# Optimization experiments

Hardware: AMD Instinct MI355X
Metric: run time of the kernel (lower is better)

The kernel has to match this reference:

```python
import jax, jax.numpy as jnp
import numpy as np

EMBED = 768
HEADS = 12


def setup_inputs() -> dict:
    key = jax.random.key(0)
    k1, k2, k3 = jax.random.split(key, 3)
    B, N, E = 2, 2048, EMBED
    x = jax.random.normal(k1, (B, N, E), dtype=jnp.float32)
    w_qkv = jax.random.normal(k2, (3 * E, E), dtype=jnp.float32) * (1.0 / np.sqrt(E))
    b_qkv = jnp.zeros((3 * E,), dtype=jnp.float32)
    w_o = jax.random.normal(k3, (E, E), dtype=jnp.float32) * (1.0 / np.sqrt(E))
    b_o = jnp.zeros((E,), dtype=jnp.float32)
    return {"x": x, "w_qkv": w_qkv, "b_qkv": b_qkv, "w_o": w_o, "b_o": b_o}


def reference(x, w_qkv, b_qkv, w_o, b_o):
    B, N, E = x.shape
    H = HEADS
    d = E // H
    # fused qkv projection (torch Linear: x @ W^T + b)
    qkv = x @ w_qkv.T + b_qkv                       # [B, N, 3E]
    # Rearrange 'b n (h qkv e) -> b qkv h n e'
    qkv = qkv.reshape(B, N, H, 3, d).transpose(0, 3, 2, 1, 4)  # [B, 3, H, N, d]
    q, k, v = qkv[:, 0], qkv[:, 1], qkv[:, 2]       # each [B, H, N, d]
    scores = jnp.einsum("bhqd,bhkd->bhqk", q, k)    # [B, H, N, N]
    attn = jax.nn.softmax(scores / jnp.sqrt(jnp.float32(E)), axis=-1)
    ctx = jnp.einsum("bhqk,bhkd->bhqd", attn, v)    # [B, H, N, d]
    ctx = ctx.transpose(0, 2, 1, 3).reshape(B, N, E)  # 'b h n d -> b n (h d)'
    out = ctx @ w_o.T + b_o
    return out
```

## Files before the change

### kernel.cpp

```cpp
#include <hip/hip_runtime.h>

#define BB 2
#define NN 2048
#define EE 768
#define HH 12
#define DD 64
#define MM (BB*NN)
#define E3 (3*EE)
#define QSCALE 0.05205877280961602f

typedef __bf16 bf16x8 __attribute__((ext_vector_type(8)));
typedef float  f32x4  __attribute__((ext_vector_type(4)));
typedef unsigned short u16x8 __attribute__((ext_vector_type(8)));

#define MFMA(a,b,c) __builtin_amdgcn_mfma_f32_16x16x32_bf16(a,b,c,0,0,0)

__device__ __forceinline__ unsigned short f2bf(float f) {
    unsigned int u = __float_as_uint(f);
    u += 0x7FFFu + ((u >> 16) & 1u);
    return (unsigned short)(u >> 16);
}

typedef __attribute__((address_space(3))) unsigned int as3u32;
typedef __attribute__((address_space(1))) unsigned int as1u32;
__device__ __forceinline__ void gll16(const void* g, void* l) {
    __builtin_amdgcn_global_load_lds((const as1u32*)(uintptr_t)g,
                                     (as3u32*)(unsigned int)(uintptr_t)l, 16, 0, 0);
}

#define XB4 786432
#define WQ4 442368
#define WO4 147456
__global__ __launch_bounds__(256)
void cast3(const float* __restrict__ x, const float* __restrict__ wq,
           const float* __restrict__ wo, unsigned short* __restrict__ dst) {
    int i = blockIdx.x * 256 + threadIdx.x;
    const float* src;
    int off;
    if (i < XB4)            { src = x;  off = i; }
    else if (i < XB4+WQ4)   { src = wq; off = i - XB4; }
    else                    { src = wo; off = i - XB4 - WQ4; }
    float4 v = ((const float4*)src)[off];
    ushort4 o;
    o.x = f2bf(v.x); o.y = f2bf(v.y); o.z = f2bf(v.z); o.w = f2bf(v.w);
    ((ushort4*)dst)[i] = o;
}

__global__ __launch_bounds__(256)
void gemm_qkv(const unsigned short* __restrict__ A, const unsigned short* __restrict__ W,
              const float* __restrict__ bias,
              unsigned short* __restrict__ o0, unsigned short* __restrict__ o1,
              unsigned short* __restrict__ o2)
{
    __shared__ unsigned short As[256 * 32];
    __shared__ unsigned short Bs[128 * 32];

    const int tid = threadIdx.x;
    const int l = tid & 63;
    const int w = tid >> 6;
    const int m0 = blockIdx.x * 256;
    const int c0 = blockIdx.y * 128;
    const int wm = (w >> 1) * 128;
    const int wn = (w & 1) * 64;

    const unsigned short* a_src[4];
    const unsigned short* b_src[2];
    unsigned short* a_dst[4];
    unsigned short* b_dst[2];
    #pragma unroll
    for (int s = 0; s < 4; ++s) {
        a_src[s] = A + (size_t)(m0 + w*64 + s*16 + (l>>2)) * EE + (l&3)*8;
        a_dst[s] = &As[(w*64 + s*16) * 32];
    }
    #pragma unroll
    for (int s = 0; s < 2; ++s) {
        b_src[s] = W + (size_t)(c0 + w*32 + s*16 + (l>>2)) * EE + (l&3)*8;
        b_dst[s] = &Bs[(w*32 + s*16) * 32];
    }

    const f32x4 zero4 = {0.f, 0.f, 0.f, 0.f};
    f32x4 acc[8][4];
    #pragma unroll
    for (int i = 0; i < 8; ++i)
        #pragma unroll
        for (int j = 0; j < 4; ++j) acc[i][j] = zero4;

    for (int k0 = 0; k0 < EE; k0 += 32) {
        __syncthreads();
        #pragma unroll
        for (int s = 0; s < 4; ++s) gll16(a_src[s] + k0, a_dst[s]);
        #pragma unroll
        for (int s = 0; s < 2; ++s) gll16(b_src[s] + k0, b_dst[s]);
        __syncthreads();

        bf16x8 af[8], bf[4];
        #pragma unroll
        for (int i = 0; i < 8; ++i)
            af[i] = *(const bf16x8*)&As[(wm + 16*i + (l&15))*32 + (l>>4)*8];
        #pragma unroll
        for (int j = 0; j < 4; ++j)
            bf[j] = *(const bf16x8*)&Bs[(wn + 16*j + (l&15))*32 + (l>>4)*8];
        #pragma unroll
        for (int i = 0; i < 8; ++i)
            #pragma unroll
            for (int j = 0; j < 4; ++j)
                acc[i][j] = MFMA(af[i], bf[j], acc[i][j]);
    }

    const int sec = (c0 + wn) >> 6;
    const int hh = sec / 3;
    const int tt = sec - hh*3;
    #pragma unroll
    for (int j = 0; j < 4; ++j) {
        const int col = c0 + wn + 16*j + (l&15);
        const int dcol = 16*j + (l&15);
        const float bj = bias[col];
        #pragma unroll
        for (int i = 0; i < 8; ++i) {
            const int row0 = m0 + wm + 16*i + (l>>4)*4;
            const int b = row0 >> 11;
            const int n = row0 & (NN - 1);
            if (tt == 2) {
                ushort4 pk;
                pk.x = f2bf(acc[i][j][0] + bj);
                pk.y = f2bf(acc[i][j][1] + bj);
                pk.z = f2bf(acc[i][j][2] + bj);
                pk.w = f2bf(acc[i][j][3] + bj);
                *(ushort4*)&o2[(((size_t)b*HH + hh)*DD + dcol)*NN + n] = pk;
            } else {
                unsigned short* dst = (tt == 0) ? o0 : o1;
                #pragma unroll
                for (int r = 0; r < 4; ++r) {
                    float val = acc[i][j][r] + bj;
                    if (tt == 0) val *= QSCALE;
                    dst[(((size_t)b*HH + hh)*NN + n + r)*DD + dcol] = f2bf(val);
                }
            }
        }
    }
}

__global__ __launch_bounds__(256)
void gemm_out(const unsigned short* __restrict__ A, const unsigned short* __restrict__ W,
              const float* __restrict__ bias, float* __restrict__ of)
{
    __shared__ unsigned short As[128 * 32];
    __shared__ unsigned short Bs[128 * 32];

    const int tid = threadIdx.x;
    const int l = tid & 63;
    const int w = tid >> 6;
    const int m0 = blockIdx.x * 128;
    const int c0 = blockIdx.y * 128;
    const int wm = (w >> 1) * 64;
    const int wn = (w & 1) * 64;

    const int s0 = w * 2;
    const unsigned short* a_src0 = A + (size_t)(m0 + s0*16      + (l>>2)) * EE + (l&3)*8;
    const unsigned short* a_src1 = A + (size_t)(m0 + (s0+1)*16  + (l>>2)) * EE + (l&3)*8;
    const unsigned short* b_src0 = W + (size_t)(c0 + s0*16      + (l>>2)) * EE + (l&3)*8;
    const unsigned short* b_src1 = W + (size_t)(c0 + (s0+1)*16  + (l>>2)) * EE + (l&3)*8;
    unsigned short* a_dst0 = &As[s0*512];
    unsigned short* a_dst1 = &As[(s0+1)*512];
    unsigned short* b_dst0 = &Bs[s0*512];
    unsigned short* b_dst1 = &Bs[(s0+1)*512];

    const f32x4 zero4 = {0.f, 0.f, 0.f, 0.f};
    f32x4 acc[4][4];
    #pragma unroll
    for (int i = 0; i < 4; ++i)
        #pragma unroll
        for (int j = 0; j < 4; ++j) acc[i][j] = zero4;

    for (int k0 = 0; k0 < EE; k0 += 32) {
        __syncthreads();
        gll16(a_src0 + k0, a_dst0);
        gll16(a_src1 + k0, a_dst1);
        gll16(b_src0 + k0, b_dst0);
        gll16(b_src1 + k0, b_dst1);
        __syncthreads();

        bf16x8 af[4], bf[4];
        #pragma unroll
        for (int i = 0; i < 4; ++i)
            af[i] = *(const bf16x8*)&As[(wm + 16*i + (l&15))*32 + (l>>4)*8];
        #pragma unroll
        for (int j = 0; j < 4; ++j)
            bf[j] = *(const bf16x8*)&Bs[(wn + 16*j + (l&15))*32 + (l>>4)*8];
        #pragma unroll
        for (int i = 0; i < 4; ++i)
            #pragma unroll
            for (int j = 0; j < 4; ++j)
                acc[i][j] = MFMA(af[i], bf[j], acc[i][j]);
    }

    #pragma unroll
    for (int j = 0; j < 4; ++j) {
        const int col = c0 + wn + 16*j + (l&15);
        const float bj = bias[col];
        #pragma unroll
        for (int i = 0; i < 4; ++i) {
            #pragma unroll
            for (int r = 0; r < 4; ++r) {
                const int row = m0 + wm + 16*i + (l>>4)*4 + r;
                of[(size_t)row * EE + col] = acc[i][j][r] + bj;
            }
        }
    }
}

__global__ __launch_bounds__(256)
void attn_mfma(const unsigned short* __restrict__ Q, const unsigned short* __restrict__ K,
               const unsigned short* __restrict__ Vt_g, unsigned short* __restrict__ ctx)
{
    __shared__ unsigned short Ks[64 * 72];
    __shared__ unsigned short Vt[64 * 72];
    __shared__ unsigned short Pq[4 * 16 * 72];

    const int tid = threadIdx.x;
    const int l = tid & 63;
    const int w = tid >> 6;
    const int quad = l >> 4;
    const int lc = l & 15;

    const int id = blockIdx.x;
    const int bh = id % 24;
    const int bq = id / 24;
    const int b  = bh / 12;
    const int h  = bh - b*12;
    const size_t hb = (size_t)bh * NN * DD;

    const f32x4 zero4 = {0.f, 0.f, 0.f, 0.f};

    const int qrow = bq*64 + w*16 + lc;
    const bf16x8 qf0 = *(const bf16x8*)(Q + hb + (size_t)qrow*DD +      quad*8);
    const bf16x8 qf1 = *(const bf16x8*)(Q + hb + (size_t)qrow*DD + 32 + quad*8);

    f32x4 o[4];
    #pragma unroll
    for (int dj = 0; dj < 4; ++dj) o[dj] = zero4;
    float lsum = 0.f;

    const int srow = tid >> 2;
    const int sc = tid & 3;
    const unsigned short* kbase = K + hb + (size_t)srow*DD + sc*16;
    const unsigned short* vbase = Vt_g + ((size_t)bh*DD + srow)*NN + sc*16;
    unsigned short* ksl = &Ks[srow*72 + sc*16];
    unsigned short* vsl = &Vt[srow*72 + sc*16];

    for (int kt = 0; kt < NN/64; ++kt) {
        const unsigned short* ksrc = kbase + (size_t)kt*64*DD;
        const unsigned short* vsrc = vbase + kt*64;
        u16x8 k0 = *(const u16x8*)ksrc;
        u16x8 k1 = *(const u16x8*)(ksrc + 8);
        u16x8 v0 = *(const u16x8*)vsrc;
        u16x8 v1 = *(const u16x8*)(vsrc + 8);
        __syncthreads();
        *(u16x8*)ksl = k0;
        *(u16x8*)(ksl + 8) = k1;
        *(u16x8*)vsl = v0;
        *(u16x8*)(vsl + 8) = v1;
        __syncthreads();

        f32x4 st[4];
        #pragma unroll
        for (int jf = 0; jf < 4; ++jf) {
            bf16x8 kf0 = *(const bf16x8*)&Ks[(16*jf + lc)*72 +      quad*8];
            bf16x8 kf1 = *(const bf16x8*)&Ks[(16*jf + lc)*72 + 32 + quad*8];
            f32x4 acc0 = MFMA(kf0, qf0, zero4);
            st[jf] = MFMA(kf1, qf1, acc0);
        }

        #pragma unroll
        for (int jf = 0; jf < 4; ++jf) {
            float e0 = __builtin_amdgcn_exp2f(st[jf][0]);
            float e1 = __builtin_amdgcn_exp2f(st[jf][1]);
            float e2 = __builtin_amdgcn_exp2f(st[jf][2]);
            float e3 = __builtin_amdgcn_exp2f(st[jf][3]);
            lsum += (e0 + e1) + (e2 + e3);
            ushort4 pk;
            pk.x = f2bf(e0); pk.y = f2bf(e1); pk.z = f2bf(e2); pk.w = f2bf(e3);
            *(ushort4*)&Pq[w*1152 + lc*72 + 16*jf + quad*4] = pk;
        }

        #pragma unroll
        for (int kb = 0; kb < 2; ++kb) {
            bf16x8 pf = *(const bf16x8*)&Pq[w*1152 + lc*72 + kb*32 + quad*8];
            #pragma unroll
            for (int dj = 0; dj < 4; ++dj) {
                bf16x8 vf = *(const bf16x8*)&Vt[(16*dj + lc)*72 + kb*32 + quad*8];
                o[dj] = MFMA(vf, pf, o[dj]);
            }
        }
    }

    lsum += __shfl_xor(lsum, 16);
    lsum += __shfl_xor(lsum, 32);
    const float inv = 1.f / lsum;

    const int n = bq*64 + w*16 + lc;
    #pragma unroll
    for (int dj = 0; dj < 4; ++dj) {
        ushort4 pk;
        pk.x = f2bf(o[dj][0] * inv);
        pk.y = f2bf(o[dj][1] * inv);
        pk.z = f2bf(o[dj][2] * inv);
        pk.w = f2bf(o[dj][3] * inv);
        *(ushort4*)&ctx[((size_t)(b*NN + n))*EE + h*DD + 16*dj + quad*4] = pk;
    }
}

extern "C" void kernel_launch(void* const* d_in, const int* in_sizes, int n_in,
                              void* d_out, int out_size, void* d_ws, size_t ws_size,
                              hipStream_t stream)
{
    const float* x     = (const float*)d_in[0];
    const float* w_qkv = (const float*)d_in[1];
    const float* b_qkv = (const float*)d_in[2];
    const float* w_o   = (const float*)d_in[3];
    const float* b_o   = (const float*)d_in[4];
    float* out = (float*)d_out;

    unsigned short* wsu = (unsigned short*)d_ws;
    const size_t XB = (size_t)MM * EE;
    const size_t WQ = (size_t)E3 * EE;
    const size_t WO = (size_t)EE * EE;
    const size_t HS = (size_t)BB * HH * NN * DD;
    unsigned short* xb   = wsu;
    unsigned short* wqb  = xb  + XB;
    unsigned short* wob  = wqb + WQ;
    unsigned short* qb   = wob + WO;
    unsigned short* kb   = qb  + HS;
    unsigned short* vtb  = kb  + HS;
    unsigned short* ctxb = vtb + HS;

    cast3<<<(XB4 + WQ4 + WO4)/256, 256, 0, stream>>>(x, w_qkv, w_o, xb);

    dim3 g1(MM/256, E3/128);
    gemm_qkv<<<g1, 256, 0, stream>>>(xb, wqb, b_qkv, qb, kb, vtb);

    attn_mfma<<<768, 256, 0, stream>>>(qb, kb, vtb, ctxb);

    dim3 g3(MM/128, EE/128);
    gemm_out<<<g3, 256, 0, stream>>>(ctxb, wob, b_o, out);
}
```

Baseline: 204.5 us.

## Shrink GEMM tiles for more blocks and XOR-swizzle attention LDS layout

The QKV GEMM tile drops from 256x128 to 128x128 and the output GEMM tile from 128x128 to 64x128, which doubles the grid sizes to fill more CUs. The attention kernel replaces padded (stride 72) shared-memory rows with unpadded 64-wide rows and XOR swizzles on K, Vt and P tiles to avoid bank conflicts while using less LDS. Smaller GEMM tiles give lower arithmetic reuse per block and more global traffic.

```diff
diff --git a/kernel.cpp b/kernel.cpp
--- a/kernel.cpp
+++ b/kernel.cpp
@@ -52,56 +52,51 @@
               unsigned short* __restrict__ o0, unsigned short* __restrict__ o1,
               unsigned short* __restrict__ o2)
 {
-    __shared__ unsigned short As[256 * 32];
+    __shared__ unsigned short As[128 * 32];
     __shared__ unsigned short Bs[128 * 32];
 
     const int tid = threadIdx.x;
     const int l = tid & 63;
     const int w = tid >> 6;
-    const int m0 = blockIdx.x * 256;
+    const int m0 = blockIdx.x * 128;
     const int c0 = blockIdx.y * 128;
-    const int wm = (w >> 1) * 128;
+    const int wm = (w >> 1) * 64;
     const int wn = (w & 1) * 64;
 
-    const unsigned short* a_src[4];
-    const unsigned short* b_src[2];
-    unsigned short* a_dst[4];
-    unsigned short* b_dst[2];
-    #pragma unroll
-    for (int s = 0; s < 4; ++s) {
-        a_src[s] = A + (size_t)(m0 + w*64 + s*16 + (l>>2)) * EE + (l&3)*8;
-        a_dst[s] = &As[(w*64 + s*16) * 32];
-    }
-    #pragma unroll
-    for (int s = 0; s < 2; ++s) {
-        b_src[s] = W + (size_t)(c0 + w*32 + s*16 + (l>>2)) * EE + (l&3)*8;
-        b_dst[s] = &Bs[(w*32 + s*16) * 32];
-    }
+    const int s0 = w * 2;
+    const unsigned short* a_src0 = A + (size_t)(m0 + s0*16      + (l>>2)) * EE + (l&3)*8;
+    const unsigned short* a_src1 = A + (size_t)(m0 + (s0+1)*16  + (l>>2)) * EE + (l&3)*8;
+    const unsigned short* b_src0 = W + (size_t)(c0 + s0*16      + (l>>2)) * EE + (l&3)*8;
+    const unsigned short* b_src1 = W + (size_t)(c0 + (s0+1)*16  + (l>>2)) * EE + (l&3)*8;
+    unsigned short* a_dst0 = &As[s0*512];
+    unsigned short* a_dst1 = &As[(s0+1)*512];
+    unsigned short* b_dst0 = &Bs[s0*512];
+    unsigned short* b_dst1 = &Bs[(s0+1)*512];
 
     const f32x4 zero4 = {0.f, 0.f, 0.f, 0.f};
-    f32x4 acc[8][4];
-    #pragma unroll
-    for (int i = 0; i < 8; ++i)
+    f32x4 acc[4][4];
+    #pragma unroll
+    for (int i = 0; i < 4; ++i)
         #pragma unroll
         for (int j = 0; j < 4; ++j) acc[i][j] = zero4;
 
     for (int k0 = 0; k0 < EE; k0 += 32) {
         __syncthreads();
-        #pragma unroll
-        for (int s = 0; s < 4; ++s) gll16(a_src[s] + k0, a_dst[s]);
-        #pragma unroll
-        for (int s = 0; s < 2; ++s) gll16(b_src[s] + k0, b_dst[s]);
-        __syncthreads();
-
-        bf16x8 af[8], bf[4];
-        #pragma unroll
-        for (int i = 0; i < 8; ++i)
+        gll16(a_src0 + k0, a_dst0);
+        gll16(a_src1 + k0, a_dst1);
+        gll16(b_src0 + k0, b_dst0);
+        gll16(b_src1 + k0, b_dst1);
+        __syncthreads();
+
+        bf16x8 af[4], bf[4];
+        #pragma unroll
+        for (int i = 0; i < 4; ++i)
             af[i] = *(const bf16x8*)&As[(wm + 16*i + (l&15))*32 + (l>>4)*8];
         #pragma unroll
         for (int j = 0; j < 4; ++j)
             bf[j] = *(const bf16x8*)&Bs[(wn + 16*j + (l&15))*32 + (l>>4)*8];
         #pragma unroll
-        for (int i = 0; i < 8; ++i)
+        for (int i = 0; i < 4; ++i)
             #pragma unroll
             for (int j = 0; j < 4; ++j)
                 acc[i][j] = MFMA(af[i], bf[j], acc[i][j]);
@@ -116,7 +111,7 @@
         const int dcol = 16*j + (l&15);
         const float bj = bias[col];
         #pragma unroll
-        for (int i = 0; i < 8; ++i) {
+        for (int i = 0; i < 4; ++i) {
             const int row0 = m0 + wm + 16*i + (l>>4)*4;
             const int b = row0 >> 11;
             const int n = row0 & (NN - 1);
@@ -144,51 +139,53 @@
 void gemm_out(const unsigned short* __restrict__ A, const unsigned short* __restrict__ W,
               const float* __restrict__ bias, float* __restrict__ of)
 {
-    __shared__ unsigned short As[128 * 32];
+    __shared__ unsigned short As[64 * 32];
     __shared__ unsigned short Bs[128 * 32];
 
     const int tid = threadIdx.x;
     const int l = tid & 63;
     const int w = tid >> 6;
-    const int m0 = blockIdx.x * 128;
+    const int m0 = blockIdx.x * 64;
     const int c0 = blockIdx.y * 128;
-    const int wm = (w >> 1) * 64;
+    const int wm = (w >> 1) * 32;
     const int wn = (w & 1) * 64;
 
-    const int s0 = w * 2;
-    const unsigned short* a_src0 = A + (size_t)(m0 + s0*16      + (l>>2)) * EE + (l&3)*8;
-    const unsigned short* a_src1 = A + (size_t)(m0 + (s0+1)*16  + (l>>2)) * EE + (l&3)*8;
-    const unsigned short* b_src0 = W + (size_t)(c0 + s0*16      + (l>>2)) * EE + (l&3)*8;
-    const unsigned short* b_src1 = W + (size_t)(c0 + (s0+1)*16  + (l>>2)) * EE + (l&3)*8;
-    unsigned short* a_dst0 = &As[s0*512];
-    unsigned short* a_dst1 = &As[(s0+1)*512];
-    unsigned short* b_dst0 = &Bs[s0*512];
-    unsigned short* b_dst1 = &Bs[(s0+1)*512];
+    const unsigned short* s_src[3];
+    unsigned short* s_dst[3];
+    #pragma unroll
+    for (int s = 0; s < 3; ++s) {
+        const int ch = 3*w + s;
+        if (ch < 4) {
+            s_src[s] = A + (size_t)(m0 + ch*16 + (l>>2)) * EE + (l&3)*8;
+            s_dst[s] = &As[ch*512];
+        } else {
+            s_src[s] = W + (size_t)(c0 + (ch-4)*16 + (l>>2)) * EE + (l&3)*8;
+            s_dst[s] = &Bs[(ch-4)*512];
+        }
+    }
 
     const f32x4 zero4 = {0.f, 0.f, 0.f, 0.f};
-    f32x4 acc[4][4];
-    #pragma unroll
-    for (int i = 0; i < 4; ++i)
+    f32x4 acc[2][4];
+    #pragma unroll
+    for (int i = 0; i < 2; ++i)
         #pragma unroll
         for (int j = 0; j < 4; ++j) acc[i][j] = zero4;
 
     for (int k0 = 0; k0 < EE; k0 += 32) {
         __syncthreads();
-        gll16(a_src0 + k0, a_dst0);
-        gll16(a_src1 + k0, a_dst1);
-        gll16(b_src0 + k0, b_dst0);
-        gll16(b_src1 + k0, b_dst1);
-        __syncthreads();
-
-        bf16x8 af[4], bf[4];
-        #pragma unroll
-        for (int i = 0; i < 4; ++i)
+        #pragma unroll
+        for (int s = 0; s < 3; ++s) gll16(s_src[s] + k0, s_dst[s]);
+        __syncthreads();
+
+        bf16x8 af[2], bf[4];
+        #pragma unroll
+        for (int i = 0; i < 2; ++i)
             af[i] = *(const bf16x8*)&As[(wm + 16*i + (l&15))*32 + (l>>4)*8];
         #pragma unroll
         for (int j = 0; j < 4; ++j)
             bf[j] = *(const bf16x8*)&Bs[(wn + 16*j + (l&15))*32 + (l>>4)*8];
         #pragma unroll
-        for (int i = 0; i < 4; ++i)
+        for (int i = 0; i < 2; ++i)
             #pragma unroll
             for (int j = 0; j < 4; ++j)
                 acc[i][j] = MFMA(af[i], bf[j], acc[i][j]);
@@ -199,7 +196,7 @@
         const int col = c0 + wn + 16*j + (l&15);
         const float bj = bias[col];
         #pragma unroll
-        for (int i = 0; i < 4; ++i) {
+        for (int i = 0; i < 2; ++i) {
             #pragma unroll
             for (int r = 0; r < 4; ++r) {
                 const int row = m0 + wm + 16*i + (l>>4)*4 + r;
@@ -213,15 +210,16 @@
 void attn_mfma(const unsigned short* __restrict__ Q, const unsigned short* __restrict__ K,
                const unsigned short* __restrict__ Vt_g, unsigned short* __restrict__ ctx)
 {
-    __shared__ unsigned short Ks[64 * 72];
-    __shared__ unsigned short Vt[64 * 72];
-    __shared__ unsigned short Pq[4 * 16 * 72];
+    __shared__ unsigned short Ks[64 * 64];
+    __shared__ unsigned short Vt[64 * 64];
+    __shared__ unsigned short Pq[4 * 16 * 64];
 
     const int tid = threadIdx.x;
     const int l = tid & 63;
     const int w = tid >> 6;
     const int quad = l >> 4;
     const int lc = l & 15;
+    const int x7 = lc & 7;
 
     const int id = blockIdx.x;
     const int bh = id % 24;
@@ -245,8 +243,18 @@
     const int sc = tid & 3;
     const unsigned short* kbase = K + hb + (size_t)srow*DD + sc*16;
     const unsigned short* vbase = Vt_g + ((size_t)bh*DD + srow)*NN + sc*16;
-    unsigned short* ksl = &Ks[srow*72 + sc*16];
-    unsigned short* vsl = &Vt[srow*72 + sc*16];
+    const int c0s = ((2*sc)     ^ (srow & 7)) * 8;
+    const int c1s = ((2*sc + 1) ^ (srow & 7)) * 8;
+    unsigned short* ksl0 = &Ks[srow*64 + c0s];
+    unsigned short* ksl1 = &Ks[srow*64 + c1s];
+    unsigned short* vsl0 = &Vt[srow*64 + c0s];
+    unsigned short* vsl1 = &Vt[srow*64 + c1s];
+
+    const int chq0 = ((    quad) ^ x7) * 8;
+    const int chq1 = ((4 + quad) ^ x7) * 8;
+    const int pw = w * 1024;
+    const int prd0 = pw + lc*64 + (((      2*quad) ^ (lc & 14)) * 4);
+    const int prd1 = pw + lc*64 + (((8 +   2*quad) ^ (lc & 14)) * 4);
 
     for (int kt = 0; kt < NN/64; ++kt) {
         const unsigned short* ksrc = kbase + (size_t)kt*64*DD;
@@ -256,17 +264,17 @@
         u16x8 v0 = *(const u16x8*)vsrc;
         u16x8 v1 = *(const u16x8*)(vsrc + 8);
         __syncthreads();
-        *(u16x8*)ksl = k0;
-        *(u16x8*)(ksl + 8) = k1;
-        *(u16x8*)vsl = v0;
-        *(u16x8*)(vsl + 8) = v1;
+        *(u16x8*)ksl0 = k0;
+        *(u16x8*)ksl1 = k1;
+        *(u16x8*)vsl0 = v0;
+        *(u16x8*)vsl1 = v1;
         __syncthreads();
 
         f32x4 st[4];
         #pragma unroll
         for (int jf = 0; jf < 4; ++jf) {
-            bf16x8 kf0 = *(const bf16x8*)&Ks[(16*jf + lc)*72 +      quad*8];
-            bf16x8 kf1 = *(const bf16x8*)&Ks[(16*jf + lc)*72 + 32 + quad*8];
+            bf16x8 kf0 = *(const bf16x8*)&Ks[(16*jf + lc)*64 + chq0];
+            bf16x8 kf1 = *(const bf16x8*)&Ks[(16*jf + lc)*64 + chq1];
             f32x4 acc0 = MFMA(kf0, qf0, zero4);
             st[jf] = MFMA(kf1, qf1, acc0);
         }
@@ -280,16 +288,18 @@
             lsum += (e0 + e1) + (e2 + e3);
             ushort4 pk;
             pk.x = f2bf(e0); pk.y = f2bf(e1); pk.z = f2bf(e2); pk.w = f2bf(e3);
-            *(ushort4*)&Pq[w*1152 + lc*72 + 16*jf + quad*4] = pk;
-        }
-
-        #pragma unroll
-        for (int kb = 0; kb < 2; ++kb) {
-            bf16x8 pf = *(const bf16x8*)&Pq[w*1152 + lc*72 + kb*32 + quad*8];
+            *(ushort4*)&Pq[pw + lc*64 + (((4*jf + quad) ^ (lc & 14)) * 4)] = pk;
+        }
+
+        {
+            bf16x8 pf0 = *(const bf16x8*)&Pq[prd0];
+            bf16x8 pf1 = *(const bf16x8*)&Pq[prd1];
             #pragma unroll
             for (int dj = 0; dj < 4; ++dj) {
-                bf16x8 vf = *(const bf16x8*)&Vt[(16*dj + lc)*72 + kb*32 + quad*8];
-                o[dj] = MFMA(vf, pf, o[dj]);
+                bf16x8 vf0 = *(const bf16x8*)&Vt[(16*dj + lc)*64 + chq0];
+                bf16x8 vf1 = *(const bf16x8*)&Vt[(16*dj + lc)*64 + chq1];
+                o[dj] = MFMA(vf0, pf0, o[dj]);
+                o[dj] = MFMA(vf1, pf1, o[dj]);
             }
         }
     }
@@ -336,11 +346,11 @@
 
     cast3<<<(XB4 + WQ4 + WO4)/256, 256, 0, stream>>>(x, w_qkv, w_o, xb);
 
-    dim3 g1(MM/256, E3/128);
+    dim3 g1(MM/128, E3/128);
     gemm_qkv<<<g1, 256, 0, stream>>>(xb, wqb, b_qkv, qb, kb, vtb);
 
     attn_mfma<<<768, 256, 0, stream>>>(qb, kb, vtb, ctxb);
 
-    dim3 g3(MM/128, EE/128);
+    dim3 g3(MM/64, EE/128);
     gemm_out<<<g3, 256, 0, stream>>>(ctxb, wob, b_o, out);
 }
```

After: 173.6 us. 1.18x faster.
